# Kernel optimization log

Measured on AMD Instinct MI355X. Metric: run time of the kernel, lower is better.

The kernel has to match this reference:

```python
import jax, jax.numpy as jnp
import numpy as np

N_NODES_PER_GRAPH = 64
NUM_GRAPHS = 2048
N = NUM_GRAPHS * N_NODES_PER_GRAPH  # 131072 total nodes
E = N * 8                           # 1048576 edges
IN_DIM, H1, H2 = 64, 128, 64
OUT_DIM = (N_NODES_PER_GRAPH * N_NODES_PER_GRAPH - N_NODES_PER_GRAPH) // 2  # 2016


def setup_inputs() -> dict:
    key = jax.random.key(0)
    ks = jax.random.split(key, 16)
    s = 0.05
    x = jax.random.normal(ks[0], (N, IN_DIM), dtype=jnp.float32)
    # edges within each graph: offsets within graph + graph base offset
    src_local = jax.random.randint(ks[1], (E,), 0, N_NODES_PER_GRAPH)
    dst_local = jax.random.randint(ks[2], (E,), 0, N_NODES_PER_GRAPH)
    gid = jnp.repeat(jnp.arange(NUM_GRAPHS), E // NUM_GRAPHS) * N_NODES_PER_GRAPH
    edge_index = jnp.stack([src_local + gid, dst_local + gid]).astype(jnp.int64)
    batch = jnp.repeat(jnp.arange(NUM_GRAPHS), N_NODES_PER_GRAPH).astype(jnp.int64)
    eps = jax.random.normal(ks[3], (NUM_GRAPHS, H2), dtype=jnp.float32)
    return {
        "x": x, "edge_index": edge_index, "batch": batch, "eps": eps,
        "w1_rel": jax.random.normal(ks[4], (IN_DIM, H1)) * s,
        "b1": jnp.zeros((H1,), jnp.float32),
        "w1_root": jax.random.normal(ks[5], (IN_DIM, H1)) * s,
        "w2_rel": jax.random.normal(ks[6], (H1, H2)) * s,
        "b2": jnp.zeros((H2,), jnp.float32),
        "w2_root": jax.random.normal(ks[7], (H1, H2)) * s,
        "w3_rel": jax.random.normal(ks[8], (H1, H2)) * s,
        "b3": jnp.zeros((H2,), jnp.float32),
        "w3_root": jax.random.normal(ks[9], (H1, H2)) * s,
        "fc1_w": jax.random.normal(ks[10], (H2, H1)) * s,
        "fc1_b": jnp.zeros((H1,), jnp.float32),
        "fc2_w": jax.random.normal(ks[11], (H1, OUT_DIM)) * s,
        "fc2_b": jnp.zeros((OUT_DIM,), jnp.float32),
    }


def _graph_conv(h, src, dst, w_rel, b, w_root):
    # PyG GraphConv: out_i = W_rel @ (sum_{j in N(i)} h_j) + b + W_root @ h_i
    agg = jax.ops.segment_sum(h[src], dst, num_segments=N)  # [N, d_in]
    return agg @ w_rel + b + h @ w_root


def _segment_mean(h, seg):
    s = jax.ops.segment_sum(h, seg, num_segments=NUM_GRAPHS)
    cnt = jax.ops.segment_sum(jnp.ones((h.shape[0],), h.dtype), seg, num_segments=NUM_GRAPHS)
    return s / jnp.maximum(cnt, 1.0)[:, None]


def reference(x, edge_index, batch, eps, w1_rel, b1, w1_root, w2_rel, b2, w2_root,
              w3_rel, b3, w3_root, fc1_w, fc1_b, fc2_w, fc2_b):
    src, dst = edge_index[0], edge_index[1]
    # encode (dropout p=0.0 -> identity)
    h1 = jax.nn.relu(_graph_conv(x, src, dst, w1_rel, b1, w1_root))
    mu = _segment_mean(_graph_conv(h1, src, dst, w2_rel, b2, w2_root), batch)
    logvar = _segment_mean(_graph_conv(h1, src, dst, w3_rel, b3, w3_root), batch)
    # reparameterize with provided eps
    z = mu + eps * jnp.exp(0.5 * logvar)
    # decode
    h = jax.nn.relu(z @ fc1_w + fc1_b)
    recon = jax.nn.sigmoid(h @ fc2_w + fc2_b)
    return recon, mu, logvar
```

## Files before the change

### kernel.cpp

```cpp
#include <hip/hip_runtime.h>
#include <math.h>

#define NG 2048
#define NPG 64
#define EPG 512
#define ETOT (NG*EPG)
#define IND 64
#define H1D 128
#define H2D 64
#define OUTD 2016

typedef __attribute__((ext_vector_type(8))) short bf16x8;
typedef __attribute__((ext_vector_type(4))) float f32x4;

__device__ inline short f2b(float f) {
  union { float f; unsigned u; } v; v.f = f;
  unsigned r = (v.u + 0x7FFFu + ((v.u >> 16) & 1u)) >> 16;
  return (short)r;
}

__global__ void p_w1(const float* __restrict__ w1_rel, const float* __restrict__ w1_root,
                     short* __restrict__ WTgF) {
  const int ct = blockIdx.x;
  const int ks = threadIdx.x >> 6, l = threadIdx.x & 63;
  const int col = ct*16 + (l & 15);
  const int kb  = ks*32 + (l >> 4)*8;
  short tmp[8];
  #pragma unroll
  for (int j = 0; j < 8; ++j) {
    const int k = kb + j;
    float v = (k < 64) ? w1_rel[k*H1D + col] : w1_root[(k - 64)*H1D + col];
    tmp[j] = f2b(v);
  }
  *(uint4*)&WTgF[(size_t)((ct*4 + ks)*64 + l)*8] = *(uint4*)tmp;
}

__global__ __launch_bounds__(256, 5) void k1_encoder(
    const float* __restrict__ x, const int* __restrict__ ei,
    const short* __restrict__ WTgF, const float* __restrict__ b1,
    short* __restrict__ SVg,
    const float* __restrict__ fc2_w, const float* __restrict__ w2_rel, const float* __restrict__ w2_root,
    const float* __restrict__ w3_rel, const float* __restrict__ w3_root,
    const float* __restrict__ fc1_w,
    short* __restrict__ WF2g, short* __restrict__ W23T, short* __restrict__ fc1T)
{
  __shared__ __align__(16) char smem[32768];
  const int g = blockIdx.x;
  const int tid = threadIdx.x;

  if (g >= NG) {
    float* L = (float*)smem;
    const int bid = g - NG;
    if (bid < 63) {
      const int c0 = bid*32;
      for (int i = tid; i < 4096; i += 256) {
        int k = i >> 5, c = i & 31;
        L[k*33 + c] = fc2_w[(size_t)k*OUTD + c0 + c];
      }
      __syncthreads();
      const int tl = tid >> 7;
      const int r  = tid & 127;
      const int ks = r >> 5;
      const int lp = r & 31;
      const int ct = bid*2 + tl;
      #pragma unroll
      for (int u = 0; u < 2; ++u) {
        const int l = lp*2 + u;
        const int cl = tl*16 + (l & 15);
        const int kb = ks*32 + (l >> 4)*8;
        short tmp[8];
        #pragma unroll
        for (int j = 0; j < 8; ++j) tmp[j] = f2b(L[(kb + j)*33 + cl]);
        *(uint4*)&WF2g[(size_t)((ct*4 + ks)*64 + l)*8] = *(uint4*)tmp;
      }
    } else if (bid < 67) {
      const int cc = bid - 63;
      const int j0 = cc*32;
      const float* wrel  = (cc < 2) ? w2_rel  : w3_rel;
      const float* wroot = (cc < 2) ? w2_root : w3_root;
      const int jl = j0 & 63;
      const int c = tid >> 3, k0 = (tid & 7)*32;
      for (int i = tid; i < 4096; i += 256) {
        int k = i >> 5, cc2 = i & 31;
        L[k*33 + cc2] = wrel[k*H2D + jl + cc2];
      }
      __syncthreads();
      if (k0 < 128)
        for (int kk = 0; kk < 32; ++kk)
          W23T[(size_t)(j0 + c)*264 + k0 + kk] = f2b(L[(k0 + kk)*33 + c]);
      __syncthreads();
      for (int i = tid; i < 4096; i += 256) {
        int k = i >> 5, cc2 = i & 31;
        L[k*33 + cc2] = wroot[k*H2D + jl + cc2];
      }
      __syncthreads();
      if (k0 >= 128)
        for (int kk = 0; kk < 32; ++kk)
          W23T[(size_t)(j0 + c)*264 + k0 + kk] = f2b(L[(k0 + kk - 128)*33 + c]);
    } else {
      const int c0 = (bid - 67)*64;
      for (int i = tid; i < 4096; i += 256) {
        int k = i >> 6, c = i & 63;
        L[k*65 + c] = fc1_w[k*H1D + c0 + c];
      }
      __syncthreads();
      const int c = tid >> 2, k0 = (tid & 3)*16;
      for (int kk = 0; kk < 16; ++kk)
        fc1T[(size_t)(c0 + c)*72 + k0 + kk] = f2b(L[(k0 + kk)*65 + c]);
    }
    return;
  }

  short* Xb   = (short*)smem;
  short* XbT  = (short*)(smem + 9216);
  short* Ab   = (short*)(smem + 18432);
  unsigned* Au32 = (unsigned*)(smem + 27648);
  float* hsum = (float*)(smem + 31744);
  float* wsum = (float*)(smem + 32256);

  const int w = tid >> 6, l = tid & 63;

  const int e0 = g*EPG + tid*2;
  const int s0 = ei[e0] & 63,     d0 = ei[ETOT + e0] & 63;
  const int s1 = ei[e0 + 1] & 63, d1 = ei[ETOT + e0 + 1] & 63;

  for (int i = tid; i < 64*16; i += 256) Au32[i] = 0u;
  if (tid < 128) { hsum[tid] = 0.f; wsum[tid] = 0.f; }

  {
    const int n = tid >> 2, f0 = (tid & 3) * 16;
    const float* xr = x + (size_t)g*(NPG*IND) + n*IND + f0;
    float4 v0 = *(const float4*)&xr[0];
    float4 v1 = *(const float4*)&xr[4];
    float4 v2 = *(const float4*)&xr[8];
    float4 v3 = *(const float4*)&xr[12];
    short b[16];
    b[0]=f2b(v0.x); b[1]=f2b(v0.y); b[2]=f2b(v0.z); b[3]=f2b(v0.w);
    b[4]=f2b(v1.x); b[5]=f2b(v1.y); b[6]=f2b(v1.z); b[7]=f2b(v1.w);
    b[8]=f2b(v2.x); b[9]=f2b(v2.y); b[10]=f2b(v2.z); b[11]=f2b(v2.w);
    b[12]=f2b(v3.x); b[13]=f2b(v3.y); b[14]=f2b(v3.z); b[15]=f2b(v3.w);
    short* xbp = &Xb[n*72 + f0];
    #pragma unroll
    for (int j = 0; j < 16; ++j) xbp[j] = b[j];
    #pragma unroll
    for (int j = 0; j < 16; ++j) XbT[(f0 + j)*72 + n] = b[j];
  }
  __syncthreads();

  atomicAdd(&Au32[d0*16 + (s0 >> 2)], 1u << (8*(s0 & 3)));
  atomicAdd(&Au32[d1*16 + (s1 >> 2)], 1u << (8*(s1 & 3)));
  __syncthreads();

  {
    const int row = tid >> 2, qw = tid & 3;
    unsigned wds[4];
    #pragma unroll
    for (int q = 0; q < 4; ++q) wds[q] = Au32[row*16 + qw*4 + q];
    unsigned* abp = (unsigned*)&Ab[row*72 + qw*16];
    #pragma unroll
    for (int q = 0; q < 4; ++q) {
      unsigned wv = wds[q];
      #pragma unroll
      for (int p = 0; p < 2; ++p) {
        unsigned c0 = (wv >> (16*p)) & 255u, c1 = (wv >> (16*p + 8)) & 255u;
        abp[q*2 + p] = (unsigned)(unsigned short)f2b((float)c0)
                     | ((unsigned)(unsigned short)f2b((float)c1) << 16);
      }
    }
  }

  float dg[4];
  {
    unsigned ps = 0;
    #pragma unroll
    for (int i = 0; i < 4; ++i) ps += Au32[((l >> 2) + 16*i)*16 + 4*w + (l & 3)];
    ps += __shfl_xor(ps, 4);
    ps += __shfl_xor(ps, 8);
    ps += __shfl_xor(ps, 16);
    ps += __shfl_xor(ps, 32);
    unsigned dword = __shfl(ps, (l >> 4));
    dg[0] = (float)(dword & 255u);
    dg[1] = (float)((dword >> 8) & 255u);
    dg[2] = (float)((dword >> 16) & 255u);
    dg[3] = (float)(dword >> 24);
  }

  const int rm = w*16;
  const int fr = l & 15;
  const int koff = (l >> 4) * 8;

  f32x4 agc[4];
  #pragma unroll
  for (int t = 0; t < 4; ++t) agc[t] = (f32x4){0.f,0.f,0.f,0.f};
  #pragma unroll
  for (int ks = 0; ks < 2; ++ks) {
    bf16x8 a = *(const bf16x8*)&Ab[(rm + fr)*72 + ks*32 + koff];
    #pragma unroll
    for (int t = 0; t < 4; ++t) {
      bf16x8 b = *(const bf16x8*)&XbT[(t*16 + fr)*72 + ks*32 + koff];
      agc[t] = __builtin_amdgcn_mfma_f32_16x16x32_bf16(a, b, agc[t], 0, 0, 0);
    }
  }
  short* AGb = Ab;
  #pragma unroll
  for (int t = 0; t < 4; ++t)
    #pragma unroll
    for (int r = 0; r < 4; ++r)
      AGb[(rm + (l>>4)*4 + r)*72 + t*16 + fr] = f2b(agc[t][r]);
  __syncthreads();

  {
    bf16x8 afr[4];
    #pragma unroll
    for (int ks = 0; ks < 4; ++ks)
      afr[ks] = (ks < 2)
        ? *(const bf16x8*)&AGb[(rm + fr)*72 + ks*32 + koff]
        : *(const bf16x8*)&Xb[(rm + fr)*72 + (ks-2)*32 + koff];

    f32x4 acc[8];
    #pragma unroll
    for (int t = 0; t < 8; ++t) acc[t] = (f32x4){0.f,0.f,0.f,0.f};
    #pragma unroll
    for (int t = 0; t < 8; ++t)
      #pragma unroll
      for (int ks = 0; ks < 4; ++ks) {
        bf16x8 b = *(const bf16x8*)&WTgF[(size_t)((t*4 + ks)*64 + l)*8];
        acc[t] = __builtin_amdgcn_mfma_f32_16x16x32_bf16(afr[ks], b, acc[t], 0, 0, 0);
      }

    #pragma unroll
    for (int t = 0; t < 8; ++t) {
      const int col = t*16 + fr;
      const float bb = b1[col];
      float hs = 0.f, ws = 0.f;
      #pragma unroll
      for (int r = 0; r < 4; ++r) {
        float v = fmaxf(acc[t][r] + bb, 0.f);
        hs += v; ws += dg[r]*v;
      }
      hs += __shfl_down(hs, 32); ws += __shfl_down(ws, 32);
      hs += __shfl_down(hs, 16); ws += __shfl_down(ws, 16);
      if (l < 16) { atomicAdd(&hsum[col], hs); atomicAdd(&wsum[col], ws); }
    }
  }
  __syncthreads();

  if (tid < 128) {
    SVg[(size_t)g*256 + tid]       = f2b(wsum[tid]);
    SVg[(size_t)g*256 + 128 + tid] = f2b(hsum[tid]);
  }
}

__global__ __launch_bounds__(256) void k1b_latent(
    const short* __restrict__ SVg, const short* __restrict__ W23T,
    const float* __restrict__ b2, const float* __restrict__ b3,
    const float* __restrict__ eps, const short* __restrict__ fc1T,
    const float* __restrict__ fc1_b,
    float* __restrict__ out_mu, float* __restrict__ out_lv, short* __restrict__ hbufB)
{
  __shared__ short SV[32*264];
  __shared__ short Zt[32*72];
  const int g0 = blockIdx.x * 32;
  const int tid = threadIdx.x;
  const int w = tid >> 6, l = tid & 63;
  const int s = w >> 1;
  const int h = w & 1;
  const int fr = l & 15;
  const int koff = (l >> 4) * 8;

  {
    const uint4* src = (const uint4*)(SVg + (size_t)g0*256);
    for (int i = tid; i < 1024; i += 256) {
      int r = i >> 5, k0 = (i & 31) * 8;
      *(uint4*)&SV[r*264 + k0] = src[i];
    }
  }
  __syncthreads();

  f32x4 acc[4];
  #pragma unroll
  for (int t = 0; t < 4; ++t) acc[t] = (f32x4){0.f,0.f,0.f,0.f};
  #pragma unroll
  for (int ks = 0; ks < 8; ++ks) {
    bf16x8 a = *(const bf16x8*)&SV[(s*16 + fr)*264 + ks*32 + koff];
    #pragma unroll
    for (int j = 0; j < 2; ++j) {
      bf16x8 bm = *(const bf16x8*)&W23T[((2*h + j)*16 + fr)*264 + ks*32 + koff];
      bf16x8 bl = *(const bf16x8*)&W23T[((2*h + j + 4)*16 + fr)*264 + ks*32 + koff];
      acc[j]     = __builtin_amdgcn_mfma_f32_16x16x32_bf16(a, bm, acc[j], 0, 0, 0);
      acc[2 + j] = __builtin_amdgcn_mfma_f32_16x16x32_bf16(a, bl, acc[2 + j], 0, 0, 0);
    }
  }
  #pragma unroll
  for (int j = 0; j < 2; ++j) {
    const int col = (2*h + j)*16 + fr;
    const float bb2 = b2[col], bb3 = b3[col];
    #pragma unroll
    for (int r = 0; r < 4; ++r) {
      const int row = s*16 + (l>>4)*4 + r;
      const size_t gg = (size_t)(g0 + row);
      float mu = acc[j][r]     * (1.f/64.f) + bb2;
      float lv = acc[2 + j][r] * (1.f/64.f) + bb3;
      out_mu[gg*64 + col] = mu;
      out_lv[gg*64 + col] = lv;
      float z = mu + eps[gg*64 + col] * __expf(0.5f*lv);
      Zt[row*72 + col] = f2b(z);
    }
  }
  __syncthreads();

  f32x4 hacc[4];
  #pragma unroll
  for (int t = 0; t < 4; ++t) hacc[t] = (f32x4){0.f,0.f,0.f,0.f};
  #pragma unroll
  for (int ks = 0; ks < 2; ++ks) {
    bf16x8 a = *(const bf16x8*)&Zt[(s*16 + fr)*72 + ks*32 + koff];
    #pragma unroll
    for (int j = 0; j < 4; ++j) {
      bf16x8 b = *(const bf16x8*)&fc1T[((h*4 + j)*16 + fr)*72 + ks*32 + koff];
      hacc[j] = __builtin_amdgcn_mfma_f32_16x16x32_bf16(a, b, hacc[j], 0, 0, 0);
    }
  }
  #pragma unroll
  for (int j = 0; j < 4; ++j) {
    const int col = (h*4 + j)*16 + fr;
    const float bb = fc1_b[col];
    #pragma unroll
    for (int r = 0; r < 4; ++r) {
      const int row = s*16 + (l>>4)*4 + r;
      hbufB[(size_t)(g0 + row)*H1D + col] = f2b(fmaxf(hacc[j][r] + bb, 0.f));
    }
  }
}

__global__ __launch_bounds__(256, 4) void k2_decoder(
    const short* __restrict__ hbufB, const short* __restrict__ WF2g,
    const float* __restrict__ fc2_b, float* __restrict__ recon)
{
  __shared__ __align__(16) short Hb[64*136];
  const int bx = blockIdx.x, by = blockIdx.y;
  const int tid = threadIdx.x;
  const int w = tid >> 6, l = tid & 63;

  {
    const uint4* src = (const uint4*)(hbufB + (size_t)bx*64*H1D);
    for (int i = tid; i < 1024; i += 256) {
      int r = i >> 4, k0 = (i & 15) * 8;
      *(uint4*)&Hb[r*136 + k0] = src[i];
    }
  }
  __syncthreads();

  const int fr = l & 15;
  const int koff = (l >> 4) * 8;

  f32x4 acc[6];
  #pragma unroll
  for (int t = 0; t < 6; ++t) acc[t] = (f32x4){0.f,0.f,0.f,0.f};

  #pragma unroll
  for (int ks = 0; ks < 4; ++ks) {
    bf16x8 a = *(const bf16x8*)&Hb[(w*16 + fr)*136 + ks*32 + koff];
    #pragma unroll
    for (int t = 0; t < 6; ++t) {
      const int ct = by*6 + t;
      bf16x8 b = *(const bf16x8*)&WF2g[(size_t)((ct*4 + ks)*64 + l)*8];
      acc[t] = __builtin_amdgcn_mfma_f32_16x16x32_bf16(a, b, acc[t], 0, 0, 0);
    }
  }

  #pragma unroll
  for (int t = 0; t < 6; ++t) {
    const int col = by*96 + t*16 + fr;
    const float bb = fc2_b[col];
    #pragma unroll
    for (int r = 0; r < 4; ++r) {
      const int row = bx*64 + w*16 + (l>>4)*4 + r;
      float v = acc[t][r] + bb;
      recon[(size_t)row*OUTD + col] = 1.f/(1.f + __expf(-v));
    }
  }
}

extern "C" void kernel_launch(void* const* d_in, const int* in_sizes, int n_in,
                              void* d_out, int out_size, void* d_ws, size_t ws_size,
                              hipStream_t stream) {
  const float* x       = (const float*)d_in[0];
  const int*   ei      = (const int*)d_in[1];
  const float* eps     = (const float*)d_in[3];
  const float* w1_rel  = (const float*)d_in[4];
  const float* b1      = (const float*)d_in[5];
  const float* w1_root = (const float*)d_in[6];
  const float* w2_rel  = (const float*)d_in[7];
  const float* b2      = (const float*)d_in[8];
  const float* w2_root = (const float*)d_in[9];
  const float* w3_rel  = (const float*)d_in[10];
  const float* b3      = (const float*)d_in[11];
  const float* w3_root = (const float*)d_in[12];
  const float* fc1_w   = (const float*)d_in[13];
  const float* fc1_b   = (const float*)d_in[14];
  const float* fc2_w   = (const float*)d_in[15];
  const float* fc2_b   = (const float*)d_in[16];

  float* recon  = (float*)d_out;
  float* out_mu = recon + (size_t)NG*OUTD;
  float* out_lv = out_mu + (size_t)NG*H2D;

  char* p = (char*)d_ws;
  short* WTgF  = (short*)p;              p += 8*4*64*8*2;
  short* WF2g  = (short*)p;              p += 126*4*64*8*2;
  short* fc1T  = (short*)p;              p += 128*72*2;
  short* W23T  = (short*)p;              p += 128*264*2;
  short* SVg   = (short*)p;              p += (size_t)NG*256*2;
  short* hbufB = (short*)p;

  p_w1<<<8, 256, 0, stream>>>(w1_rel, w1_root, WTgF);
  k1_encoder<<<NG + 69, 256, 0, stream>>>(x, ei, WTgF, b1, SVg,
      fc2_w, w2_rel, w2_root, w3_rel, w3_root, fc1_w, WF2g, W23T, fc1T);
  k1b_latent<<<64, 256, 0, stream>>>(SVg, W23T, b2, b3, eps, fc1T, fc1_b,
                                     out_mu, out_lv, hbufB);
  k2_decoder<<<dim3(32, 21), 256, 0, stream>>>(hbufB, WF2g, fc2_b, recon);
}
```

Before: 152.1 us.

## Store decoder hidden activations in MFMA fragment layout and trim encoder barriers

```diff
diff --git a/kernel.cpp b/kernel.cpp
--- a/kernel.cpp
+++ b/kernel.cpp
@@ -123,17 +123,21 @@
   const int e0 = g*EPG + tid*2;
   const int s0 = ei[e0] & 63,     d0 = ei[ETOT + e0] & 63;
   const int s1 = ei[e0 + 1] & 63, d1 = ei[ETOT + e0 + 1] & 63;
+  const int n = tid >> 2, f0 = (tid & 3) * 16;
+  const float* xr = x + (size_t)g*(NPG*IND) + n*IND + f0;
+  float4 v0 = *(const float4*)&xr[0];
+  float4 v1 = *(const float4*)&xr[4];
+  float4 v2 = *(const float4*)&xr[8];
+  float4 v3 = *(const float4*)&xr[12];
 
   for (int i = tid; i < 64*16; i += 256) Au32[i] = 0u;
   if (tid < 128) { hsum[tid] = 0.f; wsum[tid] = 0.f; }
+  __syncthreads();
+
+  atomicAdd(&Au32[d0*16 + (s0 >> 2)], 1u << (8*(s0 & 3)));
+  atomicAdd(&Au32[d1*16 + (s1 >> 2)], 1u << (8*(s1 & 3)));
 
   {
-    const int n = tid >> 2, f0 = (tid & 3) * 16;
-    const float* xr = x + (size_t)g*(NPG*IND) + n*IND + f0;
-    float4 v0 = *(const float4*)&xr[0];
-    float4 v1 = *(const float4*)&xr[4];
-    float4 v2 = *(const float4*)&xr[8];
-    float4 v3 = *(const float4*)&xr[12];
     short b[16];
     b[0]=f2b(v0.x); b[1]=f2b(v0.y); b[2]=f2b(v0.z); b[3]=f2b(v0.w);
     b[4]=f2b(v1.x); b[5]=f2b(v1.y); b[6]=f2b(v1.z); b[7]=f2b(v1.w);
@@ -145,10 +149,6 @@
     #pragma unroll
     for (int j = 0; j < 16; ++j) XbT[(f0 + j)*72 + n] = b[j];
   }
-  __syncthreads();
-
-  atomicAdd(&Au32[d0*16 + (s0 >> 2)], 1u << (8*(s0 & 3)));
-  atomicAdd(&Au32[d1*16 + (s1 >> 2)], 1u << (8*(s1 & 3)));
   __syncthreads();
 
   {
@@ -207,7 +207,6 @@
     #pragma unroll
     for (int r = 0; r < 4; ++r)
       AGb[(rm + (l>>4)*4 + r)*72 + t*16 + fr] = f2b(agc[t][r]);
-  __syncthreads();
 
   {
     bf16x8 afr[4];
@@ -256,7 +255,7 @@
     const float* __restrict__ b2, const float* __restrict__ b3,
     const float* __restrict__ eps, const short* __restrict__ fc1T,
     const float* __restrict__ fc1_b,
-    float* __restrict__ out_mu, float* __restrict__ out_lv, short* __restrict__ hbufB)
+    float* __restrict__ out_mu, float* __restrict__ out_lv, short* __restrict__ hbufF)
 {
   __shared__ short SV[32*264];
   __shared__ short Zt[32*72];
@@ -324,35 +323,34 @@
   #pragma unroll
   for (int j = 0; j < 4; ++j) {
     const int col = (h*4 + j)*16 + fr;
+    const int ks  = col >> 5;
+    const int q   = (col >> 3) & 3;
+    const int j8  = col & 7;
     const float bb = fc1_b[col];
     #pragma unroll
     for (int r = 0; r < 4; ++r) {
       const int row = s*16 + (l>>4)*4 + r;
-      hbufB[(size_t)(g0 + row)*H1D + col] = f2b(fmaxf(hacc[j][r] + bb, 0.f));
-    }
-  }
-}
-
-__global__ __launch_bounds__(256, 4) void k2_decoder(
-    const short* __restrict__ hbufB, const short* __restrict__ WF2g,
+      const int rt  = blockIdx.x*2 + (row >> 4);
+      const int lane = (row & 15) + 16*q;
+      hbufF[(size_t)((rt*4 + ks)*64 + lane)*8 + j8] = f2b(fmaxf(hacc[j][r] + bb, 0.f));
+    }
+  }
+}
+
+__global__ __launch_bounds__(256, 8) void k2_decoder(
+    const short* __restrict__ hbufF, const short* __restrict__ WF2g,
     const float* __restrict__ fc2_b, float* __restrict__ recon)
 {
-  __shared__ __align__(16) short Hb[64*136];
   const int bx = blockIdx.x, by = blockIdx.y;
   const int tid = threadIdx.x;
   const int w = tid >> 6, l = tid & 63;
-
-  {
-    const uint4* src = (const uint4*)(hbufB + (size_t)bx*64*H1D);
-    for (int i = tid; i < 1024; i += 256) {
-      int r = i >> 4, k0 = (i & 15) * 8;
-      *(uint4*)&Hb[r*136 + k0] = src[i];
-    }
-  }
-  __syncthreads();
-
   const int fr = l & 15;
-  const int koff = (l >> 4) * 8;
+  const int rt = bx*4 + w;
+
+  bf16x8 afr[4];
+  #pragma unroll
+  for (int ks = 0; ks < 4; ++ks)
+    afr[ks] = *(const bf16x8*)&hbufF[(size_t)((rt*4 + ks)*64 + l)*8];
 
   f32x4 acc[6];
   #pragma unroll
@@ -360,12 +358,11 @@
 
   #pragma unroll
   for (int ks = 0; ks < 4; ++ks) {
-    bf16x8 a = *(const bf16x8*)&Hb[(w*16 + fr)*136 + ks*32 + koff];
     #pragma unroll
     for (int t = 0; t < 6; ++t) {
       const int ct = by*6 + t;
       bf16x8 b = *(const bf16x8*)&WF2g[(size_t)((ct*4 + ks)*64 + l)*8];
-      acc[t] = __builtin_amdgcn_mfma_f32_16x16x32_bf16(a, b, acc[t], 0, 0, 0);
+      acc[t] = __builtin_amdgcn_mfma_f32_16x16x32_bf16(afr[ks], b, acc[t], 0, 0, 0);
     }
   }
 
@@ -412,12 +409,12 @@
   short* fc1T  = (short*)p;              p += 128*72*2;
   short* W23T  = (short*)p;              p += 128*264*2;
   short* SVg   = (short*)p;              p += (size_t)NG*256*2;
-  short* hbufB = (short*)p;
+  short* hbufF = (short*)p;
 
   p_w1<<<8, 256, 0, stream>>>(w1_rel, w1_root, WTgF);
   k1_encoder<<<NG + 69, 256, 0, stream>>>(x, ei, WTgF, b1, SVg,
       fc2_w, w2_rel, w2_root, w3_rel, w3_root, fc1_w, WF2g, W23T, fc1T);
   k1b_latent<<<64, 256, 0, stream>>>(SVg, W23T, b2, b3, eps, fc1T, fc1_b,
-                                     out_mu, out_lv, hbufB);
-  k2_decoder<<<dim3(32, 21), 256, 0, stream>>>(hbufB, WF2g, fc2_b, recon);
-}
+                                     out_mu, out_lv, hbufF);
+  k2_decoder<<<dim3(32, 21), 256, 0, stream>>>(hbufF, WF2g, fc2_b, recon);
+}
```

Result: faster. 145.8 us (-4.1%).
